# Kernel optimization log

Hardware: AMD Instinct MI355X
Metric: run time of the kernel (lower is better)

## Reference

```python
import jax, jax.numpy as jnp
import numpy as np

B, S, HN, TN = 8, 32, 64, 512
HID, EMB, VOCAB = 512, 512, 10000


def setup_inputs():
    key = jax.random.key(0)
    k = jax.random.split(key, 14)
    w = lambda kk, shape: jax.random.normal(kk, shape, jnp.float32) * 0.02
    return {
        "dec_out": jax.random.normal(k[0], (B, S, HID), jnp.float32),
        "history": jax.random.normal(k[1], (B, HID), jnp.float32),
        "head": jax.random.randint(k[2], (B, HN), 0, VOCAB),
        "tail": jax.random.randint(k[3], (B, TN), 0, VOCAB),
        "adj_mask": jax.random.randint(k[4], (B, HN, TN), 0, 2).astype(bool),
        "dup_mask": jax.random.randint(k[5], (B, S, TN), 0, 2).astype(bool),
        "emb_table": w(k[6], (VOCAB, EMB)),
        "W_tq": w(k[7], (2 * HID + EMB, HID)),
        "b_tq": jnp.zeros((HID,), jnp.float32),
        "W_tk": w(k[8], (EMB, HID)),
        "b_tk": jnp.zeros((HID,), jnp.float32),
        "W_tout": w(k[9], (2 * HID, HID)),
        "W_hq": w(k[10], (2 * HID, HID)),
        "b_hq": jnp.zeros((HID,), jnp.float32),
        "W_hk": w(k[11], (HID, HID)),
        "b_hk": jnp.zeros((HID,), jnp.float32),
    }


def reference(dec_out, history, head, tail, adj_mask, dup_mask, emb_table,
              W_tq, b_tq, W_tk, b_tk, W_tout, W_hq, b_hq, W_hk, b_hk):
    head_emb = emb_table[head]  # (B, HN, EMB)
    tail_emb = emb_table[tail]  # (B, TN, EMB)

    # --- tail attention query: Linear(cat([dec_out, history, head_emb])) + ELU.
    # Same math as the torch broadcast-concat, computed as a sum of three
    # partial matmuls to avoid materializing the (B,S,HN,2*hid+emb) concat.
    Wd, Wh, We = W_tq[:HID], W_tq[HID:2 * HID], W_tq[2 * HID:]
    tq = jax.nn.elu((dec_out @ Wd)[:, :, None, :]
                    + (history @ Wh)[:, None, None, :]
                    + (head_emb @ We)[:, None, :, :]
                    + b_tq)                       # (B, S, HN, HID)
    tq = tq.reshape(B, S * HN, HID)
    tk = jax.nn.elu(tail_emb @ W_tk + b_tk)       # (B, TN, HID)  (dropout=eval)

    # combined logical mask: allowed = adjacency AND not-duplicate
    mask = (adj_mask[:, None, :, :] & ~dup_mask[:, :, None, :]).reshape(B, S * HN, TN)

    # GlobalAttention (dot): score -> mask -> softmax -> context -> tanh(linear_out([c;q]))
    scores = jnp.einsum('bqh,bth->bqt', tq, tk)   # (B, S*HN, TN)
    tail_attn = jax.nn.softmax(jnp.where(mask, scores, -jnp.inf), axis=-1)
    ctx = jnp.einsum('bqt,bth->bqh', tail_attn, tk)
    graph_hid = jnp.tanh(ctx @ W_tout[:HID] + tq @ W_tout[HID:])
    graph_hid = graph_hid.reshape(B * S, HN, HID)
    tail_attn = tail_attn.reshape(B * S, HN, TN)

    # --- head attention (one-step), length-masked over HN
    hq = jax.nn.elu(dec_out @ W_hq[:HID] + (history @ W_hq[HID:])[:, None, :] + b_hq)
    hq = hq.reshape(B * S, HID)
    hk = jax.nn.elu(jnp.einsum('nkh,hd->nkd', graph_hid, W_hk) + b_hk)
    lengths = jnp.repeat(jnp.sum(head != 0, axis=-1), S)          # (B*S,)
    hscores = jnp.einsum('nh,nkh->nk', hq, hk)                    # (B*S, HN)
    lmask = jnp.arange(HN)[None, :] < lengths[:, None]
    head_attn = jax.nn.softmax(jnp.where(lmask, hscores, -jnp.inf), axis=-1)
    # (head-attention context output is discarded by the original module)

    prob = jnp.einsum('nk,nkt->nt', head_attn, tail_attn).reshape(B, S, TN)
    return jnp.log(prob + 1e-20)
```

## Files before the change

kernel.cpp:

```cpp
#include <hip/hip_runtime.h>
#include <math.h>

#define BB 8
#define SS 32
#define HN 64
#define TN 512
#define HID 512

typedef __attribute__((ext_vector_type(8))) short short8;
typedef __attribute__((ext_vector_type(4))) float f32x4;

__device__ __forceinline__ float eluf(float x) { return x > 0.f ? x : (expf(x) - 1.f); }

__device__ __forceinline__ short f2bs(float f) {
    union { float f; unsigned int u; } v; v.f = f;
    unsigned int r = v.u + 0x7fffu + ((v.u >> 16) & 1u);
    return (short)(r >> 16);
}
__device__ __forceinline__ float b2f(short s) {
    union { unsigned int u; float f; } v;
    v.u = ((unsigned int)(unsigned short)s) << 16;
    return v.f;
}

__device__ __forceinline__ void gld16(const void* g, void* l) {
    __builtin_amdgcn_global_load_lds(
        (const __attribute__((address_space(1))) void*)g,
        (__attribute__((address_space(3))) void*)l, 16, 0, 0);
}

template <int ACT, int OUTB>
__device__ __forceinline__ void gcore(
    const short* __restrict__ A, const short* __restrict__ B,
    const float* __restrict__ bias, void* __restrict__ Cv,
    int ldc, int K, int m0, int n0, int cm0, short* Ls)
{
    short* Al = Ls;
    short* Bl = Ls + 8192;
    const int tid  = threadIdx.x;
    const int lane = tid & 63;
    const int w    = tid >> 6;
    const int wr   = w >> 1, wc = w & 1;
    const int l16  = lane & 15, quad = lane >> 4;

    const int srow = w * 16 + (lane >> 2);
    const int scol = (lane & 3) * 8;

    f32x4 acc[4][4];
#pragma unroll
    for (int i = 0; i < 4; ++i)
#pragma unroll
        for (int j = 0; j < 4; ++j) { acc[i][j][0]=0.f; acc[i][j][1]=0.f; acc[i][j][2]=0.f; acc[i][j][3]=0.f; }

    short* lA = Al + w * 512;
    short* lB = Bl + w * 512;
    const long rstep = (long)64 * K;

    const short* Ag = A + (long)(m0 + srow) * K + scol;
    const short* Bg = B + (long)(n0 + srow) * K + scol;
    for (int kt = 0; kt < K; kt += 64) {
        __syncthreads();
        gld16(Ag + kt, lA);
        gld16(Ag + kt + rstep, lA + 2048);
        gld16(Ag + kt + 32, lA + 4096);
        gld16(Ag + kt + 32 + rstep, lA + 4096 + 2048);
        gld16(Bg + kt, lB);
        gld16(Bg + kt + rstep, lB + 2048);
        gld16(Bg + kt + 32, lB + 4096);
        gld16(Bg + kt + 32 + rstep, lB + 4096 + 2048);
        __syncthreads();
#pragma unroll
        for (int h = 0; h < 2; ++h) {
            short8 af[4], bf4[4];
#pragma unroll
            for (int mi = 0; mi < 4; ++mi)
                af[mi] = *(const short8*)(Al + h * 4096 + (wr * 64 + mi * 16 + l16) * 32 + quad * 8);
#pragma unroll
            for (int ni = 0; ni < 4; ++ni)
                bf4[ni] = *(const short8*)(Bl + h * 4096 + (wc * 64 + ni * 16 + l16) * 32 + quad * 8);
#pragma unroll
            for (int mi = 0; mi < 4; ++mi)
#pragma unroll
                for (int ni = 0; ni < 4; ++ni)
                    acc[mi][ni] = __builtin_amdgcn_mfma_f32_16x16x32_bf16(af[mi], bf4[ni], acc[mi][ni], 0, 0, 0);
        }
    }

    __syncthreads();

    float bv[4];
#pragma unroll
    for (int ni = 0; ni < 4; ++ni)
        bv[ni] = bias ? bias[n0 + wc * 64 + ni * 16 + l16] : 0.f;

    if (OUTB == 1) {
        short* eb = Ls + w * 1152;
        const int er = lane >> 2;
        const int ec = (lane & 3) * 16;
#pragma unroll
        for (int mi = 0; mi < 4; ++mi) {
#pragma unroll
            for (int ni = 0; ni < 4; ++ni)
#pragma unroll
                for (int r = 0; r < 4; ++r) {
                    float x = acc[mi][ni][r] + bv[ni];
                    if (ACT == 1) x = eluf(x);
                    eb[(quad * 4 + r) * 72 + ni * 16 + l16] = f2bs(x);
                }
            __builtin_amdgcn_sched_barrier(0);
            short8 v0 = *(const short8*)&eb[er * 72 + ec];
            short8 v1 = *(const short8*)&eb[er * 72 + ec + 8];
            long cb = (long)(cm0 + wr * 64 + mi * 16 + er) * ldc + n0 + wc * 64 + ec;
            *(short8*)((short*)Cv + cb)     = v0;
            *(short8*)((short*)Cv + cb + 8) = v1;
            __builtin_amdgcn_sched_barrier(0);
        }
    } else {
#pragma unroll
        for (int mi = 0; mi < 4; ++mi)
#pragma unroll
            for (int ni = 0; ni < 4; ++ni) {
                int gc = n0 + wc * 64 + ni * 16 + l16;
#pragma unroll
                for (int r = 0; r < 4; ++r) {
                    float x = acc[mi][ni][r] + bv[ni];
                    if (ACT == 1) x = eluf(x);
                    ((float*)Cv)[(long)(cm0 + wr * 64 + mi * 16 + quad * 4 + r) * ldc + gc] = x;
                }
            }
    }
}

__device__ __forceinline__ void tgemm512(
    const short* __restrict__ Arows, const short* __restrict__ B,
    short* Ls, f32x4 (&acc)[4][4])
{
    const int tid  = threadIdx.x;
    const int lane = tid & 63;
    const int w    = tid >> 6;
    const int l16  = lane & 15, quad = lane >> 4;
    short* Al = Ls;
    short* Bl = Ls + 2048;

    for (int kt = 0; kt < 512; kt += 32) {
        __syncthreads();
        if (tid < 256)
            gld16(Arows + (long)(tid >> 2) * 512 + kt + (tid & 3) * 8, Al + w * 512);
#pragma unroll
        for (int j = 0; j < 4; ++j) {
            int lin = j * 512 + tid;
            gld16(B + (long)(lin >> 2) * 512 + kt + (lin & 3) * 8, Bl + j * 4096 + w * 512);
        }
        __syncthreads();
        short8 af[4], bf[4];
#pragma unroll
        for (int mi = 0; mi < 4; ++mi)
            af[mi] = *(const short8*)(Al + (mi * 16 + l16) * 32 + quad * 8);
#pragma unroll
        for (int ni = 0; ni < 4; ++ni)
            bf[ni] = *(const short8*)(Bl + (w * 64 + ni * 16 + l16) * 32 + quad * 8);
#pragma unroll
        for (int mi = 0; mi < 4; ++mi)
#pragma unroll
            for (int ni = 0; ni < 4; ++ni)
                acc[mi][ni] = __builtin_amdgcn_mfma_f32_16x16x32_bf16(af[mi], bf[ni], acc[mi][ni], 0, 0, 0);
    }
}

template <int ACT>
__device__ __forceinline__ void epi64(
    f32x4 (&acc)[4][4], short* Ls, short* __restrict__ Crows)
{
    const int tid  = threadIdx.x;
    const int lane = tid & 63;
    const int w    = tid >> 6;
    const int l16  = lane & 15, quad = lane >> 4;
    short* eb = Ls + w * 1152;
    const int er = lane >> 2;
    const int ec = (lane & 3) * 16;
#pragma unroll
    for (int mi = 0; mi < 4; ++mi) {
#pragma unroll
        for (int ni = 0; ni < 4; ++ni)
#pragma unroll
            for (int r = 0; r < 4; ++r) {
                float x = acc[mi][ni][r];
                if (ACT == 2) x = tanhf(x);
                eb[(quad * 4 + r) * 72 + ni * 16 + l16] = f2bs(x);
            }
        __builtin_amdgcn_sched_barrier(0);
        short8 v0 = *(const short8*)&eb[er * 72 + ec];
        short8 v1 = *(const short8*)&eb[er * 72 + ec + 8];
        long cb = (long)(mi * 16 + er) * 512 + w * 64 + ec;
        *(short8*)(Crows + cb)     = v0;
        *(short8*)(Crows + cb + 8) = v1;
        __builtin_amdgcn_sched_barrier(0);
    }
}

__global__ __launch_bounds__(512, 1) void tail_kernel(
    const short* __restrict__ tqb, const short* __restrict__ tkb,
    const short* __restrict__ tkWTb, const short* __restrict__ WT,
    const int* __restrict__ adj, const int* __restrict__ dup,
    const int* __restrict__ head, const float* __restrict__ b_hk,
    const float* __restrict__ hqf,
    short* __restrict__ scb, short* __restrict__ Pb,
    float* __restrict__ out)
{
    __shared__ short Ls[20480];
    const int tid  = threadIdx.x;
    const int lane = tid & 63;
    const int w    = tid >> 6;
    const int l16  = lane & 15, quad = lane >> 4;

    const int n  = blockIdx.x;
    const int b  = n >> 5;
    const int s  = n & 31;
    const long rb = (long)n * 64;

    const short* tqrows = tqb + rb * 512;
    const short* tkb_b  = tkb + (long)b * 262144;
    const short* tkWT_b = tkWTb + (long)b * 262144;
    const short* WT7    = WT + (size_t)7 * 262144;
    const short* WT8    = WT + (size_t)8 * 262144;
    short* scrows = scb + rb * 512;
    short* Prows  = Pb  + rb * 512;

    f32x4 acc[4][4];
#pragma unroll
    for (int i = 0; i < 4; ++i)
#pragma unroll
        for (int j = 0; j < 4; ++j) { acc[i][j][0]=0.f; acc[i][j][1]=0.f; acc[i][j][2]=0.f; acc[i][j][3]=0.f; }

    tgemm512(tqrows, tkb_b, Ls, acc);
    __syncthreads();
    epi64<0>(acc, Ls, scrows);
    __syncthreads();

    for (int j = 0; j < 8; ++j) {
        int row = w * 8 + j;
        const short* srow = scrows + (long)row * 512 + lane * 8;
        const int* adjr = adj + ((long)(b * 64 + row)) * 512 + lane * 8;
        const int* dupr = dup + ((long)(b * 32 + s)) * 512 + lane * 8;
        short8 v8 = *(const short8*)srow;
        int4 a0 = *(const int4*)adjr, a1 = *(const int4*)(adjr + 4);
        int4 d0 = *(const int4*)dupr, d1 = *(const int4*)(dupr + 4);
        int am[8] = {a0.x, a0.y, a0.z, a0.w, a1.x, a1.y, a1.z, a1.w};
        int dm[8] = {d0.x, d0.y, d0.z, d0.w, d1.x, d1.y, d1.z, d1.w};
        float v[8];
        float m = -INFINITY;
#pragma unroll
        for (int i = 0; i < 8; ++i) {
            v[i] = (am[i] && !dm[i]) ? b2f(v8[i]) : -INFINITY;
            m = fmaxf(m, v[i]);
        }
#pragma unroll
        for (int d = 32; d >= 1; d >>= 1) m = fmaxf(m, __shfl_xor(m, d));
        float sum = 0.f;
#pragma unroll
        for (int i = 0; i < 8; ++i) {
            float e = (m == -INFINITY) ? 0.f : expf(v[i] - m);
            v[i] = e; sum += e;
        }
#pragma unroll
        for (int d = 32; d >= 1; d >>= 1) sum += __shfl_xor(sum, d);
        float inv = sum > 0.f ? 1.f / sum : 0.f;
        short8 o;
#pragma unroll
        for (int i = 0; i < 8; ++i) o[i] = f2bs(v[i] * inv);
        *(short8*)(Prows + (long)row * 512 + lane * 8) = o;
    }

#pragma unroll
    for (int i = 0; i < 4; ++i)
#pragma unroll
        for (int j = 0; j < 4; ++j) { acc[i][j][0]=0.f; acc[i][j][1]=0.f; acc[i][j][2]=0.f; acc[i][j][3]=0.f; }
    tgemm512(Prows, tkWT_b, Ls, acc);
    tgemm512(tqrows, WT7, Ls, acc);
    __syncthreads();
    epi64<2>(acc, Ls, scrows);

#pragma unroll
    for (int i = 0; i < 4; ++i)
#pragma unroll
        for (int j = 0; j < 4; ++j) { acc[i][j][0]=0.f; acc[i][j][1]=0.f; acc[i][j][2]=0.f; acc[i][j][3]=0.f; }
    tgemm512(scrows, WT8, Ls, acc);
    __syncthreads();

    float* redf  = (float*)Ls;
    float* hal   = (float*)Ls + 512;
    float* partf = (float*)Ls + 576;
    {
        float bv[4], hqv[4];
#pragma unroll
        for (int ni = 0; ni < 4; ++ni) {
            int col = w * 64 + ni * 16 + l16;
            bv[ni]  = b_hk[col];
            hqv[ni] = hqf[(long)n * 512 + col];
        }
#pragma unroll
        for (int mi = 0; mi < 4; ++mi)
#pragma unroll
            for (int r = 0; r < 4; ++r) {
                float p = 0.f;
#pragma unroll
                for (int ni = 0; ni < 4; ++ni)
                    p += eluf(acc[mi][ni][r] + bv[ni]) * hqv[ni];
                p += __shfl_xor(p, 1);
                p += __shfl_xor(p, 2);
                p += __shfl_xor(p, 4);
                p += __shfl_xor(p, 8);
                if (l16 == 0) redf[w * 64 + mi * 16 + quad * 4 + r] = p;
            }
    }
    __syncthreads();

    if (tid < 64) {
        float sv_raw = 0.f;
#pragma unroll
        for (int w2 = 0; w2 < 8; ++w2) sv_raw += redf[w2 * 64 + tid];
        int hv = head[b * 64 + tid];
        unsigned long long ball = __ballot(hv != 0);
        int len = __popcll(ball);
        float sv = (tid < len) ? sv_raw : -INFINITY;
        float m = sv;
#pragma unroll
        for (int d = 32; d >= 1; d >>= 1) m = fmaxf(m, __shfl_xor(m, d));
        float e = expf(sv - m);
        float sum = e;
#pragma unroll
        for (int d = 32; d >= 1; d >>= 1) sum += __shfl_xor(sum, d);
        hal[tid] = e / sum;
    }
    __syncthreads();

    {
        const short* tab = Prows + (long)(w * 8) * 512 + lane * 8;
        float a2[8] = {};
#pragma unroll
        for (int k = 0; k < 8; ++k) {
            float a = hal[w * 8 + k];
            short8 tv = *(const short8*)(tab + (long)k * 512);
#pragma unroll
            for (int u = 0; u < 8; ++u) a2[u] += a * b2f(tv[u]);
        }
        float4* pp = (float4*)&partf[w * 512 + lane * 8];
        pp[0] = make_float4(a2[0], a2[1], a2[2], a2[3]);
        pp[1] = make_float4(a2[4], a2[5], a2[6], a2[7]);
    }
    __syncthreads();

    {
        float a = 0.f;
#pragma unroll
        for (int w2 = 0; w2 < 8; ++w2) a += partf[w2 * 512 + tid];
        out[(long)n * 512 + tid] = logf(a + 1e-20f);
    }
}

struct WTDesc { const float* src[9]; short* dst[9]; };

__global__ __launch_bounds__(256) void prep(
    const float* __restrict__ dec_out, const float* __restrict__ history,
    short* __restrict__ decb,
    const float* __restrict__ emb, const int* __restrict__ head, const int* __restrict__ tail,
    short* __restrict__ embAll, WTDesc wd)
{
    __shared__ float t[32][33];
    const int id = blockIdx.x, tid = threadIdx.x;
    if (id < 132) {
        int i = (id * 256 + tid) * 4;
        float4 v = (i < 131072) ? *(const float4*)(dec_out + i)
                                : *(const float4*)(history + (i - 131072));
        short4 o;
        o.x = f2bs(v.x); o.y = f2bs(v.y); o.z = f2bs(v.z); o.w = f2bs(v.w);
        *(short4*)(decb + i) = o;
    } else if (id < 132 + 2304) {
        int r = (id - 132) * 2 + (tid >> 7);
        int c4 = (tid & 127) * 4;
        int idx = (r < 512) ? head[r] : tail[r - 512];
        float4 v = *(const float4*)(emb + (long)idx * 512 + c4);
        short4 o;
        o.x = f2bs(v.x); o.y = f2bs(v.y); o.z = f2bs(v.z); o.w = f2bs(v.w);
        *(short4*)(embAll + (long)r * 512 + c4) = o;
    } else {
        int q = id - 2436;
        int z = q >> 8, xy = q & 255;
        int x = xy & 15, y = xy >> 4;
        const float* src = wd.src[z];
        short* dst = wd.dst[z];
        int k0 = y * 32, n0 = x * 32;
        int tx = tid & 31, ty = tid >> 5;
#pragma unroll
        for (int i = 0; i < 32; i += 8)
            t[ty + i][tx] = src[(long)(k0 + ty + i) * 512 + n0 + tx];
        __syncthreads();
#pragma unroll
        for (int i = 0; i < 32; i += 8)
            dst[(long)(n0 + ty + i) * 512 + k0 + tx] = f2bs(t[tx][ty + i]);
    }
}

__global__ __launch_bounds__(256) void mgemm_multi(
    const short* __restrict__ decb, const short* __restrict__ WTall, float* __restrict__ qall,
    const short* __restrict__ embAll, const short* __restrict__ WTe, float* __restrict__ qe,
    const short* __restrict__ WTk, const float* __restrict__ b_tk, short* __restrict__ tkb)
{
    __shared__ short Ls[16384];
    int id = blockIdx.x;
    if (id < 48) {
        int y = id >> 4, x = id & 15;
        gcore<0, 0>(decb, WTall, nullptr, qall, 2048, 512, y * 128, x * 128, y * 128, Ls);
    } else if (id < 64) {
        int id2 = id - 48, y = id2 >> 2, x = id2 & 3;
        gcore<0, 0>(embAll, WTe, nullptr, qe, 512, 512, y * 128, x * 128, y * 128, Ls);
    } else {
        int id3 = id - 64, y = id3 >> 2, x = id3 & 3;
        gcore<1, 1>(embAll, WTk, b_tk, tkb, 512, 512, 512 + y * 128, x * 128, y * 128, Ls);
    }
}

__global__ __launch_bounds__(256) void l3_kernel(
    const float* __restrict__ qall, const float* __restrict__ qe,
    const float* __restrict__ b_tq, short* __restrict__ tqb,
    const short* __restrict__ WTo1, const short* __restrict__ tkb, short* __restrict__ tkWTb,
    const float* __restrict__ b_hq, float* __restrict__ hqf)
{
    __shared__ short Ls[16384];
    if (blockIdx.x < 8192) {
        long gid = (long)blockIdx.x * 256 + threadIdx.x;
        int r = (int)(gid >> 7), j0 = ((int)gid & 127) * 4;
        int b = r >> 11, rem = r & 2047, s = rem >> 6, h = rem & 63;
        float4 d = *(const float4*)(qall + (long)(b * 32 + s) * 2048 + j0);
        float4 q = *(const float4*)(qall + (long)(256 + b) * 2048 + 1024 + j0);
        float4 e = *(const float4*)(qe + (long)(b * 64 + h) * 512 + j0);
        float4 bb = *(const float4*)(b_tq + j0);
        short4 o;
        o.x = f2bs(eluf(d.x + q.x + e.x + bb.x));
        o.y = f2bs(eluf(d.y + q.y + e.y + bb.y));
        o.z = f2bs(eluf(d.z + q.z + e.z + bb.z));
        o.w = f2bs(eluf(d.w + q.w + e.w + bb.w));
        *(short4*)(tqb + (long)r * 512 + j0) = o;
    } else if (blockIdx.x < 8320) {
        int id2 = blockIdx.x - 8192;
        int z = id2 >> 4, r = id2 & 15;
        int x = r & 3, y = r >> 2;
        gcore<0, 1>(WTo1, tkb + (long)z * 262144, nullptr,
                    tkWTb + (long)z * 262144, 512, 512, y * 128, x * 128, y * 128, Ls);
    } else {
        long gid = (long)(blockIdx.x - 8320) * 256 + threadIdx.x;
        int n = (int)(gid >> 7), j0 = ((int)gid & 127) * 4;
        int b = n >> 5;
        float4 d = *(const float4*)(qall + (long)n * 2048 + 512 + j0);
        float4 h2 = *(const float4*)(qall + (long)(256 + b) * 2048 + 1536 + j0);
        float4 bb = *(const float4*)(b_hq + j0);
        float4 o;
        o.x = eluf(d.x + h2.x + bb.x);
        o.y = eluf(d.y + h2.y + bb.y);
        o.z = eluf(d.z + h2.z + bb.z);
        o.w = eluf(d.w + h2.w + bb.w);
        *(float4*)(hqf + (long)n * 512 + j0) = o;
    }
}

extern "C" void kernel_launch(void* const* d_in, const int* in_sizes, int n_in,
                              void* d_out, int out_size, void* d_ws, size_t ws_size,
                              hipStream_t stream)
{
    const float* dec_out = (const float*)d_in[0];
    const float* history = (const float*)d_in[1];
    const int*   head    = (const int*)d_in[2];
    const int*   tail    = (const int*)d_in[3];
    const int*   adj     = (const int*)d_in[4];
    const int*   dup     = (const int*)d_in[5];
    const float* emb     = (const float*)d_in[6];
    const float* W_tq    = (const float*)d_in[7];
    const float* b_tq    = (const float*)d_in[8];
    const float* W_tk    = (const float*)d_in[9];
    const float* b_tk    = (const float*)d_in[10];
    const float* W_tout  = (const float*)d_in[11];
    const float* W_hq    = (const float*)d_in[12];
    const float* b_hq    = (const float*)d_in[13];
    const float* W_hk    = (const float*)d_in[14];
    const float* b_hk    = (const float*)d_in[15];
    float* out = (float*)d_out;

    char* ws = (char*)d_ws;
    auto alloc = [&](size_t bytes) -> void* {
        char* p = ws;
        ws += (bytes + 255) & ~(size_t)255;
        return (void*)p;
    };
    short* decb   = (short*)alloc((size_t)384 * 512 * 2);
    short* embAll = (short*)alloc((size_t)4608 * 512 * 2);
    short* WT     = (short*)alloc((size_t)9 * 512 * 512 * 2);
    float* qall   = (float*)alloc((size_t)384 * 2048 * 4);
    float* qe     = (float*)alloc((size_t)512 * 512 * 4);
    float* hqf    = (float*)alloc((size_t)256 * 512 * 4);
    short* tkb    = (short*)alloc((size_t)4096 * 512 * 2);
    short* tkWTb  = (short*)alloc((size_t)4096 * 512 * 2);
    short* tqb    = (short*)alloc((size_t)16384 * 512 * 2);
    short* scb    = (short*)alloc((size_t)16384 * 512 * 2);
    short* Pb     = (short*)alloc((size_t)16384 * 512 * 2);

    WTDesc wd;
    wd.src[0] = W_tq;               wd.dst[0] = WT;
    wd.src[1] = W_hq;               wd.dst[1] = WT + (size_t)1 * 262144;
    wd.src[2] = W_tq + 512 * 512;   wd.dst[2] = WT + (size_t)2 * 262144;
    wd.src[3] = W_hq + 512 * 512;   wd.dst[3] = WT + (size_t)3 * 262144;
    wd.src[4] = W_tq + 1024 * 512;  wd.dst[4] = WT + (size_t)4 * 262144;
    wd.src[5] = W_tk;               wd.dst[5] = WT + (size_t)5 * 262144;
    wd.src[6] = W_tout;             wd.dst[6] = WT + (size_t)6 * 262144;
    wd.src[7] = W_tout + 512 * 512; wd.dst[7] = WT + (size_t)7 * 262144;
    wd.src[8] = W_hk;               wd.dst[8] = WT + (size_t)8 * 262144;

    prep<<<4740, 256, 0, stream>>>(dec_out, history, decb, emb, head, tail, embAll, wd);
    mgemm_multi<<<192, 256, 0, stream>>>(decb, WT, qall, embAll, WT + (size_t)4 * 262144, qe,
                                         WT + (size_t)5 * 262144, b_tk, tkb);
    l3_kernel<<<8448, 256, 0, stream>>>(qall, qe, b_tq, tqb, WT + (size_t)6 * 262144, tkb, tkWTb,
                                        b_hq, hqf);
    tail_kernel<<<256, 512, 0, stream>>>(tqb, tkb, tkWTb, WT, adj, dup, head, b_hk, hqf,
                                         scb, Pb, out);
}
```

Before: 230.2 us.

## Fuse tq/hq construction into tail kernel and keep tq resident in LDS

Moves the elementwise construction of tq (ELU of summed partial projections) and hq into the tail kernel, storing the 64x512 tq tile in a swizzled LDS buffer instead of writing and re-reading a 16 MB global tq array. Scores and graph_hid intermediates also stay in LDS rather than going through global scratch. The GEMM loop becomes double-buffered, with explicit vmcnt waits and XOR-swizzled layouts meant to avoid bank conflicts. The block index is remapped so neighbouring blocks spread across batches. This removes large global round-trips and one kernel's worth of elementwise work, at the cost of about 160 KB of LDS per block and more fragile manual synchronisation.

```diff
diff --git a/kernel.cpp b/kernel.cpp
--- a/kernel.cpp
+++ b/kernel.cpp
@@ -131,7 +131,15 @@
     }
 }
 
-__device__ __forceinline__ void tgemm512(
+#define L_TQ   0
+#define L_BST  32768
+#define L_AST  65536
+#define L_EB   69632
+#define L_HQ   78848
+#define L_TOT  79872
+
+template <int AFT>
+__device__ __forceinline__ void tgemmv(
     const short* __restrict__ Arows, const short* __restrict__ B,
     short* Ls, f32x4 (&acc)[4][4])
 {
@@ -139,43 +147,81 @@
     const int lane = tid & 63;
     const int w    = tid >> 6;
     const int l16  = lane & 15, quad = lane >> 4;
-    short* Al = Ls;
-    short* Bl = Ls + 2048;
-
-    for (int kt = 0; kt < 512; kt += 32) {
-        __syncthreads();
-        if (tid < 256)
-            gld16(Arows + (long)(tid >> 2) * 512 + kt + (tid & 3) * 8, Al + w * 512);
+    short* TQ  = Ls + L_TQ;
+    short* BST = Ls + L_BST;
+    short* AST = Ls + L_AST;
+
+    auto STAGE = [&](int kt, int p) {
+        short* Bl = BST + p * 16384;
 #pragma unroll
         for (int j = 0; j < 4; ++j) {
             int lin = j * 512 + tid;
-            gld16(B + (long)(lin >> 2) * 512 + kt + (lin & 3) * 8, Bl + j * 4096 + w * 512);
-        }
-        __syncthreads();
+            int r = lin >> 2, gs = lin & 3;
+            int g = gs ^ ((r >> 1) & 3);
+            gld16(B + (long)r * 512 + kt + g * 8, Bl + j * 4096 + w * 512);
+        }
+        if constexpr (AFT == 0) {
+            if (tid < 256) {
+                short* Al = AST + p * 2048;
+                int r = tid >> 2, gs = tid & 3;
+                int g = gs ^ ((r >> 1) & 3);
+                gld16(Arows + (long)r * 512 + kt + g * 8, Al + w * 512);
+            }
+        }
+    };
+
+    STAGE(0, 0);
+    int p = 0;
+    for (int kt = 0; kt < 512; kt += 32, p ^= 1) {
+        if (kt + 32 < 512) {
+            STAGE(kt + 32, p ^ 1);
+            if (AFT == 0 && w < 4) asm volatile("s_waitcnt vmcnt(5)" ::: "memory");
+            else                   asm volatile("s_waitcnt vmcnt(4)" ::: "memory");
+        } else {
+            asm volatile("s_waitcnt vmcnt(0)" ::: "memory");
+        }
+        __builtin_amdgcn_s_barrier();
+        __builtin_amdgcn_sched_barrier(0);
+
+        short* Bl = BST + p * 16384;
         short8 af[4], bf[4];
 #pragma unroll
-        for (int mi = 0; mi < 4; ++mi)
-            af[mi] = *(const short8*)(Al + (mi * 16 + l16) * 32 + quad * 8);
-#pragma unroll
-        for (int ni = 0; ni < 4; ++ni)
-            bf[ni] = *(const short8*)(Bl + (w * 64 + ni * 16 + l16) * 32 + quad * 8);
+        for (int mi = 0; mi < 4; ++mi) {
+            int row = mi * 16 + l16;
+            if constexpr (AFT == 1) {
+                int slot = ((kt >> 3) + quad) ^ (row & 7);
+                af[mi] = *(const short8*)(TQ + row * 512 + slot * 8);
+            } else {
+                short* Al = AST + p * 2048;
+                int slot = quad ^ ((row >> 1) & 3);
+                af[mi] = *(const short8*)(Al + row * 32 + slot * 8);
+            }
+        }
+#pragma unroll
+        for (int ni = 0; ni < 4; ++ni) {
+            int row = w * 64 + ni * 16 + l16;
+            int slot = quad ^ ((row >> 1) & 3);
+            bf[ni] = *(const short8*)(Bl + row * 32 + slot * 8);
+        }
 #pragma unroll
         for (int mi = 0; mi < 4; ++mi)
 #pragma unroll
             for (int ni = 0; ni < 4; ++ni)
                 acc[mi][ni] = __builtin_amdgcn_mfma_f32_16x16x32_bf16(af[mi], bf[ni], acc[mi][ni], 0, 0, 0);
-    }
-}
-
-template <int ACT>
-__device__ __forceinline__ void epi64(
-    f32x4 (&acc)[4][4], short* Ls, short* __restrict__ Crows)
+        asm volatile("s_waitcnt lgkmcnt(0)" ::: "memory");
+        __builtin_amdgcn_s_barrier();
+        __builtin_amdgcn_sched_barrier(0);
+    }
+}
+
+template <int MODE>
+__device__ __forceinline__ void epi(f32x4 (&acc)[4][4], short* Ls)
 {
     const int tid  = threadIdx.x;
     const int lane = tid & 63;
     const int w    = tid >> 6;
     const int l16  = lane & 15, quad = lane >> 4;
-    short* eb = Ls + w * 1152;
+    short* eb = Ls + L_EB + w * 1152;
     const int er = lane >> 2;
     const int ec = (lane & 3) * 16;
 #pragma unroll
@@ -185,46 +231,85 @@
 #pragma unroll
             for (int r = 0; r < 4; ++r) {
                 float x = acc[mi][ni][r];
-                if (ACT == 2) x = tanhf(x);
+                if (MODE == 1) x = tanhf(x);
                 eb[(quad * 4 + r) * 72 + ni * 16 + l16] = f2bs(x);
             }
         __builtin_amdgcn_sched_barrier(0);
         short8 v0 = *(const short8*)&eb[er * 72 + ec];
         short8 v1 = *(const short8*)&eb[er * 72 + ec + 8];
-        long cb = (long)(mi * 16 + er) * 512 + w * 64 + ec;
-        *(short8*)(Crows + cb)     = v0;
-        *(short8*)(Crows + cb + 8) = v1;
+        int row = mi * 16 + er;
+        if (MODE == 0) {
+            short* SC = Ls + L_BST;
+            *(short8*)(SC + row * 512 + w * 64 + ec)     = v0;
+            *(short8*)(SC + row * 512 + w * 64 + ec + 8) = v1;
+        } else {
+            int g0 = (w * 64 + ec) >> 3;
+            *(short8*)(Ls + L_TQ + row * 512 + ((g0)     ^ (row & 7)) * 8) = v0;
+            *(short8*)(Ls + L_TQ + row * 512 + ((g0 + 1) ^ (row & 7)) * 8) = v1;
+        }
         __builtin_amdgcn_sched_barrier(0);
     }
 }
 
 __global__ __launch_bounds__(512, 1) void tail_kernel(
-    const short* __restrict__ tqb, const short* __restrict__ tkb,
-    const short* __restrict__ tkWTb, const short* __restrict__ WT,
+    const float* __restrict__ qall, const float* __restrict__ qe,
+    const float* __restrict__ b_tq, const float* __restrict__ b_hq,
+    const short* __restrict__ tkb, const short* __restrict__ tkWTb,
+    const short* __restrict__ WT,
     const int* __restrict__ adj, const int* __restrict__ dup,
     const int* __restrict__ head, const float* __restrict__ b_hk,
-    const float* __restrict__ hqf,
-    short* __restrict__ scb, short* __restrict__ Pb,
-    float* __restrict__ out)
-{
-    __shared__ short Ls[20480];
+    short* __restrict__ Pb, float* __restrict__ out)
+{
+    __shared__ short Ls[L_TOT];
     const int tid  = threadIdx.x;
     const int lane = tid & 63;
     const int w    = tid >> 6;
     const int l16  = lane & 15, quad = lane >> 4;
 
-    const int n  = blockIdx.x;
-    const int b  = n >> 5;
-    const int s  = n & 31;
+    const int n = (blockIdx.x & 7) * 32 + (blockIdx.x >> 3);
+    const int b = n >> 5;
+    const int s = n & 31;
     const long rb = (long)n * 64;
 
-    const short* tqrows = tqb + rb * 512;
     const short* tkb_b  = tkb + (long)b * 262144;
     const short* tkWT_b = tkWTb + (long)b * 262144;
     const short* WT7    = WT + (size_t)7 * 262144;
     const short* WT8    = WT + (size_t)8 * 262144;
-    short* scrows = scb + rb * 512;
-    short* Prows  = Pb  + rb * 512;
+    short* Prows = Pb + rb * 512;
+    float* HQ = (float*)(Ls + L_HQ);
+
+    {
+        const int cg = tid & 63;
+        const int wg = tid >> 6;
+        float4 qd0 = *(const float4*)(qall + (long)n * 2048 + cg * 8);
+        float4 qd1 = *(const float4*)(qall + (long)n * 2048 + cg * 8 + 4);
+        float4 qh0 = *(const float4*)(qall + (long)(256 + b) * 2048 + 1024 + cg * 8);
+        float4 qh1 = *(const float4*)(qall + (long)(256 + b) * 2048 + 1024 + cg * 8 + 4);
+        float4 bt0 = *(const float4*)(b_tq + cg * 8);
+        float4 bt1 = *(const float4*)(b_tq + cg * 8 + 4);
+        float base[8] = {qd0.x + qh0.x + bt0.x, qd0.y + qh0.y + bt0.y,
+                         qd0.z + qh0.z + bt0.z, qd0.w + qh0.w + bt0.w,
+                         qd1.x + qh1.x + bt1.x, qd1.y + qh1.y + bt1.y,
+                         qd1.z + qh1.z + bt1.z, qd1.w + qh1.w + bt1.w};
+#pragma unroll
+        for (int i = 0; i < 8; ++i) {
+            int h = wg * 8 + i;
+            const float* er = qe + (long)(b * 64 + h) * 512 + cg * 8;
+            float4 e0 = *(const float4*)er;
+            float4 e1 = *(const float4*)(er + 4);
+            float ev[8] = {e0.x, e0.y, e0.z, e0.w, e1.x, e1.y, e1.z, e1.w};
+            short8 o;
+#pragma unroll
+            for (int u = 0; u < 8; ++u) o[u] = f2bs(eluf(base[u] + ev[u]));
+            int slot = cg ^ (h & 7);
+            *(short8*)(Ls + L_TQ + h * 512 + slot * 8) = o;
+        }
+        if (tid < 512) {
+            HQ[tid] = eluf(qall[(long)n * 2048 + 512 + tid]
+                         + qall[(long)(256 + b) * 2048 + 1536 + tid] + b_hq[tid]);
+        }
+    }
+    __syncthreads();
 
     f32x4 acc[4][4];
 #pragma unroll
@@ -232,71 +317,73 @@
 #pragma unroll
         for (int j = 0; j < 4; ++j) { acc[i][j][0]=0.f; acc[i][j][1]=0.f; acc[i][j][2]=0.f; acc[i][j][3]=0.f; }
 
-    tgemm512(tqrows, tkb_b, Ls, acc);
-    __syncthreads();
-    epi64<0>(acc, Ls, scrows);
-    __syncthreads();
-
-    for (int j = 0; j < 8; ++j) {
-        int row = w * 8 + j;
-        const short* srow = scrows + (long)row * 512 + lane * 8;
-        const int* adjr = adj + ((long)(b * 64 + row)) * 512 + lane * 8;
+    tgemmv<1>(nullptr, tkb_b, Ls, acc);
+    epi<0>(acc, Ls);
+    __syncthreads();
+
+    {
+        short* SC = Ls + L_BST;
         const int* dupr = dup + ((long)(b * 32 + s)) * 512 + lane * 8;
-        short8 v8 = *(const short8*)srow;
-        int4 a0 = *(const int4*)adjr, a1 = *(const int4*)(adjr + 4);
         int4 d0 = *(const int4*)dupr, d1 = *(const int4*)(dupr + 4);
-        int am[8] = {a0.x, a0.y, a0.z, a0.w, a1.x, a1.y, a1.z, a1.w};
         int dm[8] = {d0.x, d0.y, d0.z, d0.w, d1.x, d1.y, d1.z, d1.w};
-        float v[8];
-        float m = -INFINITY;
-#pragma unroll
-        for (int i = 0; i < 8; ++i) {
-            v[i] = (am[i] && !dm[i]) ? b2f(v8[i]) : -INFINITY;
-            m = fmaxf(m, v[i]);
-        }
-#pragma unroll
-        for (int d = 32; d >= 1; d >>= 1) m = fmaxf(m, __shfl_xor(m, d));
-        float sum = 0.f;
-#pragma unroll
-        for (int i = 0; i < 8; ++i) {
-            float e = (m == -INFINITY) ? 0.f : expf(v[i] - m);
-            v[i] = e; sum += e;
-        }
-#pragma unroll
-        for (int d = 32; d >= 1; d >>= 1) sum += __shfl_xor(sum, d);
-        float inv = sum > 0.f ? 1.f / sum : 0.f;
-        short8 o;
-#pragma unroll
-        for (int i = 0; i < 8; ++i) o[i] = f2bs(v[i] * inv);
-        *(short8*)(Prows + (long)row * 512 + lane * 8) = o;
-    }
+        for (int j = 0; j < 8; ++j) {
+            int row = w * 8 + j;
+            short8 v8 = *(const short8*)(SC + row * 512 + lane * 8);
+            const int* adjr = adj + ((long)(b * 64 + row)) * 512 + lane * 8;
+            int4 a0 = *(const int4*)adjr, a1 = *(const int4*)(adjr + 4);
+            int am[8] = {a0.x, a0.y, a0.z, a0.w, a1.x, a1.y, a1.z, a1.w};
+            float v[8];
+            float m = -INFINITY;
+#pragma unroll
+            for (int i = 0; i < 8; ++i) {
+                v[i] = (am[i] && !dm[i]) ? b2f(v8[i]) : -INFINITY;
+                m = fmaxf(m, v[i]);
+            }
+#pragma unroll
+            for (int d = 32; d >= 1; d >>= 1) m = fmaxf(m, __shfl_xor(m, d));
+            float sum = 0.f;
+#pragma unroll
+            for (int i = 0; i < 8; ++i) {
+                float e = (m == -INFINITY) ? 0.f : expf(v[i] - m);
+                v[i] = e; sum += e;
+            }
+#pragma unroll
+            for (int d = 32; d >= 1; d >>= 1) sum += __shfl_xor(sum, d);
+            float inv = sum > 0.f ? 1.f / sum : 0.f;
+            short8 o;
+#pragma unroll
+            for (int i = 0; i < 8; ++i) o[i] = f2bs(v[i] * inv);
+            *(short8*)(Prows + (long)row * 512 + lane * 8) = o;
+        }
+    }
+    __syncthreads();
 
 #pragma unroll
     for (int i = 0; i < 4; ++i)
 #pragma unroll
         for (int j = 0; j < 4; ++j) { acc[i][j][0]=0.f; acc[i][j][1]=0.f; acc[i][j][2]=0.f; acc[i][j][3]=0.f; }
-    tgemm512(Prows, tkWT_b, Ls, acc);
-    tgemm512(tqrows, WT7, Ls, acc);
-    __syncthreads();
-    epi64<2>(acc, Ls, scrows);
+    tgemmv<1>(nullptr, WT7, Ls, acc);
+    tgemmv<0>(Prows, tkWT_b, Ls, acc);
+    epi<1>(acc, Ls);
+    __syncthreads();
 
 #pragma unroll
     for (int i = 0; i < 4; ++i)
 #pragma unroll
         for (int j = 0; j < 4; ++j) { acc[i][j][0]=0.f; acc[i][j][1]=0.f; acc[i][j][2]=0.f; acc[i][j][3]=0.f; }
-    tgemm512(scrows, WT8, Ls, acc);
-    __syncthreads();
-
-    float* redf  = (float*)Ls;
-    float* hal   = (float*)Ls + 512;
-    float* partf = (float*)Ls + 576;
+    tgemmv<1>(nullptr, WT8, Ls, acc);
+
+    float* F     = (float*)(Ls + L_BST);
+    float* redf  = F;
+    float* hal   = F + 512;
+    float* partf = F + 576;
     {
         float bv[4], hqv[4];
 #pragma unroll
         for (int ni = 0; ni < 4; ++ni) {
             int col = w * 64 + ni * 16 + l16;
             bv[ni]  = b_hk[col];
-            hqv[ni] = hqf[(long)n * 512 + col];
+            hqv[ni] = HQ[col];
         }
 #pragma unroll
         for (int mi = 0; mi < 4; ++mi)
@@ -420,47 +507,15 @@
     }
 }
 
-__global__ __launch_bounds__(256) void l3_kernel(
-    const float* __restrict__ qall, const float* __restrict__ qe,
-    const float* __restrict__ b_tq, short* __restrict__ tqb,
-    const short* __restrict__ WTo1, const short* __restrict__ tkb, short* __restrict__ tkWTb,
-    const float* __restrict__ b_hq, float* __restrict__ hqf)
+__global__ __launch_bounds__(256) void tkwt_kernel(
+    const short* __restrict__ WTo1, const short* __restrict__ tkb, short* __restrict__ tkWTb)
 {
     __shared__ short Ls[16384];
-    if (blockIdx.x < 8192) {
-        long gid = (long)blockIdx.x * 256 + threadIdx.x;
-        int r = (int)(gid >> 7), j0 = ((int)gid & 127) * 4;
-        int b = r >> 11, rem = r & 2047, s = rem >> 6, h = rem & 63;
-        float4 d = *(const float4*)(qall + (long)(b * 32 + s) * 2048 + j0);
-        float4 q = *(const float4*)(qall + (long)(256 + b) * 2048 + 1024 + j0);
-        float4 e = *(const float4*)(qe + (long)(b * 64 + h) * 512 + j0);
-        float4 bb = *(const float4*)(b_tq + j0);
-        short4 o;
-        o.x = f2bs(eluf(d.x + q.x + e.x + bb.x));
-        o.y = f2bs(eluf(d.y + q.y + e.y + bb.y));
-        o.z = f2bs(eluf(d.z + q.z + e.z + bb.z));
-        o.w = f2bs(eluf(d.w + q.w + e.w + bb.w));
-        *(short4*)(tqb + (long)r * 512 + j0) = o;
-    } else if (blockIdx.x < 8320) {
-        int id2 = blockIdx.x - 8192;
-        int z = id2 >> 4, r = id2 & 15;
-        int x = r & 3, y = r >> 2;
-        gcore<0, 1>(WTo1, tkb + (long)z * 262144, nullptr,
-                    tkWTb + (long)z * 262144, 512, 512, y * 128, x * 128, y * 128, Ls);
-    } else {
-        long gid = (long)(blockIdx.x - 8320) * 256 + threadIdx.x;
-        int n = (int)(gid >> 7), j0 = ((int)gid & 127) * 4;
-        int b = n >> 5;
-        float4 d = *(const float4*)(qall + (long)n * 2048 + 512 + j0);
-        float4 h2 = *(const float4*)(qall + (long)(256 + b) * 2048 + 1536 + j0);
-        float4 bb = *(const float4*)(b_hq + j0);
-        float4 o;
-        o.x = eluf(d.x + h2.x + bb.x);
-        o.y = eluf(d.y + h2.y + bb.y);
-        o.z = eluf(d.z + h2.z + bb.z);
-        o.w = eluf(d.w + h2.w + bb.w);
-        *(float4*)(hqf + (long)n * 512 + j0) = o;
-    }
+    int id = blockIdx.x;
+    int z = id >> 4, r = id & 15;
+    int x = r & 3, y = r >> 2;
+    gcore<0, 1>(WTo1, tkb + (long)z * 262144, nullptr,
+                tkWTb + (long)z * 262144, 512, 512, y * 128, x * 128, y * 128, Ls);
 }
 
 extern "C" void kernel_launch(void* const* d_in, const int* in_sizes, int n_in,
@@ -496,11 +551,8 @@
     short* WT     = (short*)alloc((size_t)9 * 512 * 512 * 2);
     float* qall   = (float*)alloc((size_t)384 * 2048 * 4);
     float* qe     = (float*)alloc((size_t)512 * 512 * 4);
-    float* hqf    = (float*)alloc((size_t)256 * 512 * 4);
     short* tkb    = (short*)alloc((size_t)4096 * 512 * 2);
     short* tkWTb  = (short*)alloc((size_t)4096 * 512 * 2);
-    short* tqb    = (short*)alloc((size_t)16384 * 512 * 2);
-    short* scb    = (short*)alloc((size_t)16384 * 512 * 2);
     short* Pb     = (short*)alloc((size_t)16384 * 512 * 2);
 
     WTDesc wd;
@@ -517,8 +569,7 @@
     prep<<<4740, 256, 0, stream>>>(dec_out, history, decb, emb, head, tail, embAll, wd);
     mgemm_multi<<<192, 256, 0, stream>>>(decb, WT, qall, embAll, WT + (size_t)4 * 262144, qe,
                                          WT + (size_t)5 * 262144, b_tk, tkb);
-    l3_kernel<<<8448, 256, 0, stream>>>(qall, qe, b_tq, tqb, WT + (size_t)6 * 262144, tkb, tkWTb,
-                                        b_hq, hqf);
-    tail_kernel<<<256, 512, 0, stream>>>(tqb, tkb, tkWTb, WT, adj, dup, head, b_hk, hqf,
-                                         scb, Pb, out);
-}
+    tkwt_kernel<<<128, 256, 0, stream>>>(WT + (size_t)6 * 262144, tkb, tkWTb);
+    tail_kernel<<<256, 512, 0, stream>>>(qall, qe, b_tq, b_hq, tkb, tkWTb, WT,
+                                         adj, dup, head, b_hk, Pb, out);
+}
```

Measured after the change: 198.8 us, median of 2. 1.16x faster.
